# Optimization experiments

Measured on AMD Instinct MI355X. Metric: run time of the kernel, lower is better.

Reference implementation:

```python
import jax, jax.numpy as jnp
import numpy as np

B, T, D_IN, D, K, H, BAND = 4, 1536, 512, 512, 2, 8, 24
DH = D // H
ALPHA, BETA, EPS = 6.0, 0.5, 1e-5


def _ln(x, g, b):
    m = x.mean(-1, keepdims=True)
    v = ((x - m) ** 2).mean(-1, keepdims=True)
    return (x - m) / jnp.sqrt(v + EPS) * g + b


def setup_inputs() -> dict:
    key = jax.random.key(0)
    ks = jax.random.split(key, 16)
    sc = 0.02
    inp = {
        "x_m": jax.random.normal(ks[0], (B, T, D_IN), jnp.float32),
        "A": jax.random.uniform(ks[1], (B, T, K), jnp.float32),
        "W_in": jax.random.normal(ks[2], (D_IN, D), jnp.float32) * sc,
        "b_in": jnp.zeros((D,), jnp.float32),
        "ln_q_g": jnp.ones((D,), jnp.float32), "ln_q_b": jnp.zeros((D,), jnp.float32),
        "ln_kv_g": jnp.ones((D,), jnp.float32), "ln_kv_b": jnp.zeros((D,), jnp.float32),
        "Wq": jax.random.normal(ks[3], (D, D), jnp.float32) * sc,
        "bq": jnp.zeros((D,), jnp.float32),
        "Wk": jax.random.normal(ks[4], (D, D), jnp.float32) * sc,
        "bk": jnp.zeros((D,), jnp.float32),
        "Wv": jax.random.normal(ks[5], (D, D), jnp.float32) * sc,
        "bv": jnp.zeros((D,), jnp.float32),
        "Wo": jax.random.normal(ks[6], (D, D), jnp.float32) * sc,
        "bo": jnp.zeros((D,), jnp.float32),
        "ln_f_g": jnp.ones((D,), jnp.float32), "ln_f_b": jnp.zeros((D,), jnp.float32),
        "W1": jax.random.normal(ks[7], (D, 4 * D), jnp.float32) * sc,
        "b1": jnp.zeros((4 * D,), jnp.float32),
        "W2": jax.random.normal(ks[8], (4 * D, D), jnp.float32) * sc,
        "b2": jnp.zeros((D,), jnp.float32),
        "ln_s_g": jnp.ones((D,), jnp.float32), "ln_s_b": jnp.zeros((D,), jnp.float32),
        "spk_tags": jax.random.normal(ks[9], (K, D), jnp.float32) / np.sqrt(D),
    }
    return inp


def reference(x_m, A, W_in, b_in, ln_q_g, ln_q_b, ln_kv_g, ln_kv_b,
              Wq, bq, Wk, bk, Wv, bv, Wo, bo,
              ln_f_g, ln_f_b, W1, b1, W2, b2, ln_s_g, ln_s_b, spk_tags):
    X = x_m @ W_in + b_in                      # [B,T,D]
    W_hat = jax.nn.sigmoid(ALPHA * (A - BETA))  # [B,T,K] sigmoid gating

    # banded additive mask (|i-j| <= BAND allowed)
    idx = jnp.arange(T)
    allowed = jnp.abs(idx[:, None] - idx[None, :]) <= BAND
    mask = jnp.where(allowed, 0.0, -jnp.inf).astype(X.dtype)  # [T,T]

    # K/V come from the (shared) mixed memory X
    KV = _ln(X, ln_kv_g, ln_kv_b)
    k_p = (KV @ Wk + bk).reshape(B, T, H, DH)
    v_p = (KV @ Wv + bv).reshape(B, T, H, DH)

    streams = []
    for kk in range(K):
        Xk = X * W_hat[..., kk:kk + 1]
        Q = _ln(Xk, ln_q_g, ln_q_b)
        q = (Q @ Wq + bq).reshape(B, T, H, DH)
        scores = jnp.einsum('bthd,bshd->bhts', q, k_p) / np.sqrt(DH) + mask
        p = jax.nn.softmax(scores, axis=-1)
        y = jnp.einsum('bhts,bshd->bthd', p, v_p).reshape(B, T, D) @ Wo + bo
        y = Xk + y                              # residual after attention
        h = _ln(y, ln_f_g, ln_f_b)
        h = jax.nn.gelu(h @ W1 + b1, approximate=False) @ W2 + b2
        out_k = y + h + spk_tags[kk]            # ffn residual + speaker tag
        out_k = _ln(out_k, ln_s_g, ln_s_b)      # per-stream LayerNorm
        streams.append(out_k)
    return jnp.concatenate(streams, axis=1)    # [B, K*T, D]
```

## Files before the change

kernel.cpp:

```cpp
#include <hip/hip_runtime.h>
#include <hip/hip_bf16.h>
#include <math.h>

#define B_    4
#define T_    1536
#define DIN_  512
#define D_    512
#define K_    2
#define H_    8
#define BAND_ 24
#define DH_   64
#define M_    (B_*T_)
#define M2_   (2*M_)
#define ALPHA_ 6.0f
#define BETA_  0.5f
#define EPS_   1e-5f

using bf8  = __attribute__((ext_vector_type(8))) short;
using f32x4 = __attribute__((ext_vector_type(4))) float;

__device__ __forceinline__ void async_copy16(const void* g, void* l) {
  __builtin_amdgcn_global_load_lds(
      (const __attribute__((address_space(1))) unsigned int*)g,
      (__attribute__((address_space(3))) unsigned int*)l, 16, 0, 0);
}

__device__ __forceinline__ short f2bf(float v) {
  __hip_bfloat16 h = (__hip_bfloat16)v;
  return *(short*)&h;
}
__device__ __forceinline__ float bf2f(short s) {
  union { unsigned u; float f; } c;
  c.u = ((unsigned)(unsigned short)s) << 16;
  return c.f;
}
__device__ __forceinline__ int swz64(int row, int col) {
  return (col & ~63) | ((((col >> 3) ^ row) & 7) << 3) | (col & 7);
}
__device__ __forceinline__ float fast_gelu(float x) {
  const float t = fmaf(0.1029504013f, x * x, 2.3021170686f);
  const float e = __builtin_amdgcn_exp2f(x * t);
  const float r = __builtin_amdgcn_rcpf(e + 1.0f);
  return fmaf(-x, r, x);
}
__device__ __forceinline__ float wave_sum(float s) {
#pragma unroll
  for (int o = 1; o < 64; o <<= 1) s += __shfl_xor(s, o);
  return s;
}

template<int BM, int BN, int NI, int NJ, int FLAGS>
__global__ __launch_bounds__(256) void gemm_bt_t(
    const short* __restrict__ A, const short* __restrict__ Bt,
    const float* __restrict__ bias, const void* __restrict__ res,
    const float* __restrict__ tag2,
    void* __restrict__ Cout, int M, int N, int Kd, int gx) {
  __shared__ short lA[BM * 64];
  __shared__ short lB[BN * 64];
  const int gy   = gridDim.x / gx;
  const int xcd  = blockIdx.x & 7;
  const int seq  = blockIdx.x >> 3;
  const int rpx  = gy >> 3;
  const int by   = xcd * rpx + seq / gx;
  const int bx   = seq % gx;
  const int tid  = threadIdx.x;
  const int wave = tid >> 6, lane = tid & 63;
  const int block_m = by * BM, block_n = bx * BN;
  const int wm = (wave & 1) * (BM / 2), wn = (wave >> 1) * (BN / 2);
  const int l15 = lane & 15, quad = lane >> 4, l7 = lane & 7;
  f32x4 acc[NI][NJ] = {};

  for (int k0 = 0; k0 < Kd; k0 += 64) {
    __syncthreads();
#pragma unroll
    for (int i = 0; i < BM / 32; ++i) {
      const int cb = wave * (BM * 2) + i * 64;
      const int c  = cb + lane;
      async_copy16(A + (size_t)(block_m + (c >> 3)) * Kd + k0 + (c & 7) * 8,
                   &lA[cb * 8]);
    }
#pragma unroll
    for (int i = 0; i < BN / 32; ++i) {
      const int cb = wave * (BN * 2) + i * 64;
      const int c  = cb + lane;
      async_copy16(Bt + (size_t)(block_n + (c >> 3)) * Kd + k0 + (c & 7) * 8,
                   &lB[cb * 8]);
    }
    __syncthreads();
#pragma unroll
    for (int ks = 0; ks < 2; ++ks) {
      bf8 af[NI], bfr[NJ];
#pragma unroll
      for (int i = 0; i < NI; ++i)
        af[i] = *(const bf8*)&lA[(wm + i * 16 + l15) * 64 + (((ks * 4 + quad) ^ l7) << 3)];
#pragma unroll
      for (int j = 0; j < NJ; ++j)
        bfr[j] = *(const bf8*)&lB[(wn + j * 16 + l15) * 64 + (((ks * 4 + quad) ^ l7) << 3)];
#pragma unroll
      for (int i = 0; i < NI; ++i)
#pragma unroll
        for (int j = 0; j < NJ; ++j)
          acc[i][j] = __builtin_amdgcn_mfma_f32_16x16x32_bf16(bfr[j], af[i], acc[i][j], 0, 0, 0);
    }
  }

  const int half = M >> 1;
#pragma unroll
  for (int i = 0; i < NI; ++i) {
    const int row  = block_m + wm + i * 16 + l15;
    const size_t rowN = (size_t)row * N;
    const int toff = (row >= half) ? N : 0;
#pragma unroll
    for (int j = 0; j < NJ; ++j) {
      const int colb = block_n + wn + j * 16 + quad * 4;
      const float4 bb = *(const float4*)&bias[colb];
      float v0 = acc[i][j][0] + bb.x;
      float v1 = acc[i][j][1] + bb.y;
      float v2 = acc[i][j][2] + bb.z;
      float v3 = acc[i][j][3] + bb.w;
      if constexpr (FLAGS & 8) {
        const short4 rv = *(const short4*)&((const short*)res)[rowN + colb];
        v0 += bf2f(rv.x); v1 += bf2f(rv.y); v2 += bf2f(rv.z); v3 += bf2f(rv.w);
      }
      if constexpr (FLAGS & 16) {
        const float4 rv = *(const float4*)&((const float*)res)[rowN + colb];
        v0 += rv.x; v1 += rv.y; v2 += rv.z; v3 += rv.w;
      }
      if constexpr (FLAGS & 32) {
        const float4 tg = *(const float4*)&tag2[toff + colb];
        v0 += tg.x; v1 += tg.y; v2 += tg.z; v3 += tg.w;
      }
      if constexpr (FLAGS & 1) {
        v0 = fast_gelu(v0); v1 = fast_gelu(v1);
        v2 = fast_gelu(v2); v3 = fast_gelu(v3);
      }
      if constexpr (FLAGS & 2) {
        const int oc = (FLAGS & 4) ? swz64(row, colb) : colb;
        short4 o;
        o.x = f2bf(v0); o.y = f2bf(v1); o.z = f2bf(v2); o.w = f2bf(v3);
        *(short4*)&((short*)Cout)[rowN + oc] = o;
      } else {
        float4 o; o.x = v0; o.y = v1; o.z = v2; o.w = v3;
        *(float4*)&((float*)Cout)[rowN + colb] = o;
      }
    }
  }
}

__device__ __forceinline__ void tconv_tile(const float* __restrict__ W,
                                           short* __restrict__ Wt, int K, int N,
                                           int bx, int by, int tid, float (*s)[33]) {
  const int tx = tid & 31, ty = tid >> 5;
  const int k0 = by * 32, n0 = bx * 32;
#pragma unroll
  for (int r = 0; r < 4; ++r)
    s[ty * 4 + r][tx] = W[(size_t)(k0 + ty * 4 + r) * N + n0 + tx];
  __syncthreads();
#pragma unroll
  for (int r = 0; r < 4; ++r) {
    const int n = n0 + ty * 4 + r;
    Wt[(size_t)n * K + swz64(n, k0 + tx)] = f2bf(s[tx][ty * 4 + r]);
  }
}

__global__ __launch_bounds__(256) void prep_k(
    const float* __restrict__ x_m, short* __restrict__ xb,
    const float* __restrict__ W_in, short* __restrict__ WtIn,
    const float* __restrict__ Wq,  short* __restrict__ WtQ,
    const float* __restrict__ Wk,  const float* __restrict__ Wv,
    short* __restrict__ WtKV,
    const float* __restrict__ Wo,  short* __restrict__ WtO,
    const float* __restrict__ W1,  short* __restrict__ Wt1,
    const float* __restrict__ W2,  short* __restrict__ Wt2,
    const float* __restrict__ bk,  const float* __restrict__ bv,
    float* __restrict__ bkv) {
  __shared__ float s[32][33];
  const int blk = blockIdx.x, tid = threadIdx.x;
  if (blk < 3072) {
    const int e = (blk * 256 + tid) * 4;
    const int row = e >> 9, col = e & 511;
    const float4 v = *(const float4*)&x_m[e];
    short4 o;
    o.x = f2bf(v.x); o.y = f2bf(v.y); o.z = f2bf(v.z); o.w = f2bf(v.w);
    *(short4*)&xb[((size_t)row << 9) | swz64(row, col)] = o;
  } else if (blk < 3328) {
    const int t = blk - 3072; tconv_tile(W_in, WtIn, DIN_, D_, t & 15, t >> 4, tid, s);
  } else if (blk < 3584) {
    const int t = blk - 3328; tconv_tile(Wq, WtQ, D_, D_, t & 15, t >> 4, tid, s);
  } else if (blk < 3840) {
    const int t = blk - 3584; tconv_tile(Wk, WtKV, D_, D_, t & 15, t >> 4, tid, s);
  } else if (blk < 4096) {
    const int t = blk - 3840; tconv_tile(Wv, WtKV + (size_t)D_ * D_, D_, D_, t & 15, t >> 4, tid, s);
  } else if (blk < 4352) {
    const int t = blk - 4096; tconv_tile(Wo, WtO, D_, D_, t & 15, t >> 4, tid, s);
  } else if (blk < 5376) {
    const int t = blk - 4352; tconv_tile(W1, Wt1, D_, 4 * D_, t & 63, t >> 6, tid, s);
  } else if (blk < 6400) {
    const int t = blk - 5376; tconv_tile(W2, Wt2, 4 * D_, D_, t & 15, t >> 4, tid, s);
  } else {
    const int i = (blk - 6400) * 256 + tid;
    bkv[i] = (i < D_) ? bk[i] : bv[i - D_];
  }
}

__global__ __launch_bounds__(256) void ln_bf_k(const short* __restrict__ in,
                                               const float* __restrict__ g,
                                               const float* __restrict__ b,
                                               short* __restrict__ out) {
  const int row  = blockIdx.x * 4 + (threadIdx.x >> 6);
  const int lane = threadIdx.x & 63;
  const int c0   = lane * 8;
  const bf8 xv = *(const bf8*)&in[(size_t)row * D_ + c0];
  float v[8];
  float s = 0.0f;
#pragma unroll
  for (int e = 0; e < 8; ++e) { v[e] = bf2f(xv[e]); s += v[e]; }
  const float mean = wave_sum(s) * (1.0f / D_);
  float s2 = 0.0f;
#pragma unroll
  for (int e = 0; e < 8; ++e) { v[e] -= mean; s2 += v[e] * v[e]; }
  const float inv = rsqrtf(wave_sum(s2) * (1.0f / D_) + EPS_);
  const float4 g0 = *(const float4*)&g[c0];
  const float4 g1 = *(const float4*)&g[c0 + 4];
  const float4 b0 = *(const float4*)&b[c0];
  const float4 b1 = *(const float4*)&b[c0 + 4];
  bf8 o;
  o[0] = f2bf(v[0] * inv * g0.x + b0.x);
  o[1] = f2bf(v[1] * inv * g0.y + b0.y);
  o[2] = f2bf(v[2] * inv * g0.z + b0.z);
  o[3] = f2bf(v[3] * inv * g0.w + b0.w);
  o[4] = f2bf(v[4] * inv * g1.x + b1.x);
  o[5] = f2bf(v[5] * inv * g1.y + b1.y);
  o[6] = f2bf(v[6] * inv * g1.z + b1.z);
  o[7] = f2bf(v[7] * inv * g1.w + b1.w);
  *(bf8*)&out[(size_t)row * D_ + swz64(row, c0)] = o;
}

__global__ __launch_bounds__(256) void scale_ln_k(
    const short* __restrict__ X, const float* __restrict__ Ain,
    const float* __restrict__ g, const float* __restrict__ b,
    short* __restrict__ Xk, short* __restrict__ out) {
  const int row  = blockIdx.x * 4 + (threadIdx.x >> 6);
  const int lane = threadIdx.x & 63;
  const int c0   = lane * 8;
  const int kk = row / M_, rm = row % M_;
  const float a = Ain[(size_t)rm * K_ + kk];
  const float w = __builtin_amdgcn_rcpf(1.0f + __expf(-ALPHA_ * (a - BETA_)));
  const bf8 xv = *(const bf8*)&X[(size_t)rm * D_ + c0];
  float v[8];
  float s = 0.0f;
  bf8 xo;
#pragma unroll
  for (int e = 0; e < 8; ++e) {
    v[e] = bf2f(xv[e]) * w;
    xo[e] = f2bf(v[e]);
    s += v[e];
  }
  *(bf8*)&Xk[(size_t)row * D_ + c0] = xo;
  const float mean = wave_sum(s) * (1.0f / D_);
  float s2 = 0.0f;
#pragma unroll
  for (int e = 0; e < 8; ++e) { v[e] -= mean; s2 += v[e] * v[e]; }
  const float inv = rsqrtf(wave_sum(s2) * (1.0f / D_) + EPS_);
  const float4 g0 = *(const float4*)&g[c0];
  const float4 g1 = *(const float4*)&g[c0 + 4];
  const float4 b0 = *(const float4*)&b[c0];
  const float4 b1 = *(const float4*)&b[c0 + 4];
  bf8 o;
  o[0] = f2bf(v[0] * inv * g0.x + b0.x);
  o[1] = f2bf(v[1] * inv * g0.y + b0.y);
  o[2] = f2bf(v[2] * inv * g0.z + b0.z);
  o[3] = f2bf(v[3] * inv * g0.w + b0.w);
  o[4] = f2bf(v[4] * inv * g1.x + b1.x);
  o[5] = f2bf(v[5] * inv * g1.y + b1.y);
  o[6] = f2bf(v[6] * inv * g1.z + b1.z);
  o[7] = f2bf(v[7] * inv * g1.w + b1.w);
  *(bf8*)&out[(size_t)row * D_ + swz64(row, c0)] = o;
}

__global__ __launch_bounds__(256) void final_ln_k(
    const short* __restrict__ t2, const float* __restrict__ g,
    const float* __restrict__ b, float* __restrict__ out) {
  const int row  = blockIdx.x * 4 + (threadIdx.x >> 6);
  const int lane = threadIdx.x & 63;
  const int c0   = lane * 8;
  const int kk = row / M_, rm = row % M_;
  const int bb_ = rm / T_, t = rm % T_;
  const size_t orow = (size_t)bb_ * (K_ * T_) + (size_t)kk * T_ + t;
  const bf8 xv = *(const bf8*)&t2[(size_t)row * D_ + c0];
  float v[8];
  float s = 0.0f;
#pragma unroll
  for (int e = 0; e < 8; ++e) { v[e] = bf2f(xv[e]); s += v[e]; }
  const float mean = wave_sum(s) * (1.0f / D_);
  float s2 = 0.0f;
#pragma unroll
  for (int e = 0; e < 8; ++e) { v[e] -= mean; s2 += v[e] * v[e]; }
  const float inv = rsqrtf(wave_sum(s2) * (1.0f / D_) + EPS_);
  const float4 g0 = *(const float4*)&g[c0];
  const float4 g1 = *(const float4*)&g[c0 + 4];
  const float4 b0 = *(const float4*)&b[c0];
  const float4 b1 = *(const float4*)&b[c0 + 4];
  float4 o0, o1;
  o0.x = v[0] * inv * g0.x + b0.x;
  o0.y = v[1] * inv * g0.y + b0.y;
  o0.z = v[2] * inv * g0.z + b0.z;
  o0.w = v[3] * inv * g0.w + b0.w;
  o1.x = v[4] * inv * g1.x + b1.x;
  o1.y = v[5] * inv * g1.y + b1.y;
  o1.z = v[6] * inv * g1.z + b1.z;
  o1.w = v[7] * inv * g1.w + b1.w;
  *(float4*)&out[orow * D_ + c0]     = o0;
  *(float4*)&out[orow * D_ + c0 + 4] = o1;
}

#define QT_  64
#define KT_  (QT_ + 2 * BAND_)
#define SKQ_ 72
#define STV_ 136
__global__ __launch_bounds__(256) void attn_mfma_k(
    const short* __restrict__ q, const short* __restrict__ KVp,
    short* __restrict__ out) {
  __shared__ short sK[KT_ * SKQ_];
  __shared__ short sQ[QT_ * SKQ_];
  __shared__ short sVt[DH_ * STV_];
  __shared__ short sP[4][16 * SKQ_];
  const int t0 = blockIdx.x * QT_;
  const int h  = blockIdx.y;
  const int z  = blockIdx.z;
  const int b  = z % B_;
  const int tid = threadIdx.x;
  const int wave = tid >> 6, lane = tid & 63;
  const int rr = tid >> 5, c2 = tid & 31;

  for (int r0 = 0; r0 < KT_; r0 += 8) {
    const int r = r0 + rr;
    const int s = t0 - BAND_ + r;
    short2 kv = {0, 0}, vv = {0, 0};
    if (s >= 0 && s < T_) {
      const size_t g = (size_t)(b * T_ + s) * (2 * D_) + h * DH_ + c2 * 2;
      kv = *(const short2*)&KVp[g];
      vv = *(const short2*)&KVp[g + D_];
    }
    *(short2*)&sK[r * SKQ_ + c2 * 2] = kv;
    sVt[(c2 * 2)     * STV_ + r] = vv.x;
    sVt[(c2 * 2 + 1) * STV_ + r] = vv.y;
  }
  for (int r0 = 0; r0 < QT_; r0 += 8) {
    const int r = r0 + rr;
    const size_t g = (size_t)(z * T_ + t0 + r) * D_ + h * DH_ + c2 * 2;
    *(short2*)&sQ[r * SKQ_ + c2 * 2] = *(const short2*)&q[g];
  }
  __syncthreads();

  const int qg  = wave * 16;
  const int l15 = lane & 15, quad = lane >> 4;

  bf8 qa0 = *(const bf8*)&sQ[(qg + l15) * SKQ_ + quad * 8];
  bf8 qa1 = *(const bf8*)&sQ[(qg + l15) * SKQ_ + 32 + quad * 8];
  f32x4 acc[4];
#pragma unroll
  for (int j = 0; j < 4; ++j) {
    const bf8 kb0 = *(const bf8*)&sK[(qg + j * 16 + l15) * SKQ_ + quad * 8];
    const bf8 kb1 = *(const bf8*)&sK[(qg + j * 16 + l15) * SKQ_ + 32 + quad * 8];
    f32x4 z4 = {0.f, 0.f, 0.f, 0.f};
    acc[j] = __builtin_amdgcn_mfma_f32_16x16x32_bf16(qa0, kb0, z4, 0, 0, 0);
    acc[j] = __builtin_amdgcn_mfma_f32_16x16x32_bf16(qa1, kb1, acc[j], 0, 0, 0);
  }

#pragma unroll
  for (int reg = 0; reg < 4; ++reg) {
    const int i = quad * 4 + reg;
    float sc[4];
    float mx = -1e30f;
#pragma unroll
    for (int j = 0; j < 4; ++j) {
      const int c = j * 16 + l15;
      const int s = t0 + qg - BAND_ + c;
      const int rel = c - i;
      const bool valid = (rel >= 0) && (rel <= 2 * BAND_) && (s >= 0) && (s < T_);
      sc[j] = valid ? acc[j][reg] * 0.125f : -1e30f;
      mx = fmaxf(mx, sc[j]);
    }
    for (int o = 1; o < 16; o <<= 1) mx = fmaxf(mx, __shfl_xor(mx, o));
    float p[4], se = 0.0f;
#pragma unroll
    for (int j = 0; j < 4; ++j) {
      p[j] = (sc[j] > -1e29f) ? __expf(sc[j] - mx) : 0.0f;
      se += p[j];
    }
    for (int o = 1; o < 16; o <<= 1) se += __shfl_xor(se, o);
    const float inv = __builtin_amdgcn_rcpf(se);
#pragma unroll
    for (int j = 0; j < 4; ++j)
      sP[wave][i * SKQ_ + j * 16 + l15] = f2bf(p[j] * inv);
  }

  const bf8 pa0 = *(const bf8*)&sP[wave][l15 * SKQ_ + quad * 8];
  const bf8 pa1 = *(const bf8*)&sP[wave][l15 * SKQ_ + 32 + quad * 8];
  f32x4 oacc[4] = {};
#pragma unroll
  for (int dt = 0; dt < 4; ++dt) {
    const bf8 vb0 = *(const bf8*)&sVt[(dt * 16 + l15) * STV_ + qg + quad * 8];
    const bf8 vb1 = *(const bf8*)&sVt[(dt * 16 + l15) * STV_ + qg + 32 + quad * 8];
    oacc[dt] = __builtin_amdgcn_mfma_f32_16x16x32_bf16(pa0, vb0, oacc[dt], 0, 0, 0);
    oacc[dt] = __builtin_amdgcn_mfma_f32_16x16x32_bf16(pa1, vb1, oacc[dt], 0, 0, 0);
  }
#pragma unroll
  for (int dt = 0; dt < 4; ++dt)
#pragma unroll
    for (int reg = 0; reg < 4; ++reg) {
      const int i = quad * 4 + reg;
      const int row = t0 + qg + i;
      const int col = h * DH_ + dt * 16 + l15;
      out[(size_t)(z * T_ + row) * D_ + swz64(row, col)] = f2bf(oacc[dt][reg]);
    }
}

extern "C" void kernel_launch(void* const* d_in, const int* in_sizes, int n_in,
                              void* d_out, int out_size, void* d_ws, size_t ws_size,
                              hipStream_t stream) {
  const float* x_m    = (const float*)d_in[0];
  const float* A      = (const float*)d_in[1];
  const float* W_in   = (const float*)d_in[2];
  const float* b_in   = (const float*)d_in[3];
  const float* ln_q_g = (const float*)d_in[4];
  const float* ln_q_b = (const float*)d_in[5];
  const float* ln_kv_g= (const float*)d_in[6];
  const float* ln_kv_b= (const float*)d_in[7];
  const float* Wq     = (const float*)d_in[8];
  const float* bq     = (const float*)d_in[9];
  const float* Wk     = (const float*)d_in[10];
  const float* bk     = (const float*)d_in[11];
  const float* Wv     = (const float*)d_in[12];
  const float* bv     = (const float*)d_in[13];
  const float* Wo     = (const float*)d_in[14];
  const float* bo     = (const float*)d_in[15];
  const float* ln_f_g = (const float*)d_in[16];
  const float* ln_f_b = (const float*)d_in[17];
  const float* W1     = (const float*)d_in[18];
  const float* b1     = (const float*)d_in[19];
  const float* W2     = (const float*)d_in[20];
  const float* b2     = (const float*)d_in[21];
  const float* ln_s_g = (const float*)d_in[22];
  const float* ln_s_b = (const float*)d_in[23];
  const float* tags   = (const float*)d_in[24];
  float* out = (float*)d_out;

  const size_t MD = (size_t)M_ * D_;
  float* bkv = (float*)d_ws;
  short* X    = (short*)(bkv + 1024);
  short* Xk2  = X    + MD;
  short* LNb2 = Xk2  + 2 * MD;
  short* qb2  = LNb2 + 2 * MD;
  short* KVpb = qb2  + 2 * MD;
  short* T2b  = KVpb + 2 * MD;
  short* H1b  = T2b  + 2 * MD;
  short* WtIn = H1b + (size_t)M2_ * 4 * D_;
  short* WtQ  = WtIn + (size_t)D_ * DIN_;
  short* WtKV = WtQ  + (size_t)D_ * D_;
  short* WtO  = WtKV + (size_t)2 * D_ * D_;
  short* Wt1  = WtO  + (size_t)D_ * D_;
  short* Wt2  = Wt1  + (size_t)4 * D_ * D_;
  short* xb   = qb2;
  short* KVb  = LNb2;

  prep_k<<<6404, 256, 0, stream>>>(x_m, xb, W_in, WtIn, Wq, WtQ, Wk, Wv, WtKV,
                                   Wo, WtO, W1, Wt1, W2, Wt2, bk, bv, bkv);

  gemm_bt_t<128,64,4,2, 2><<<(D_/64) * (M_/128), 256, 0, stream>>>(
      xb, WtIn, b_in, nullptr, nullptr, X, M_, D_, DIN_, D_/64);
  ln_bf_k<<<M_/4, 256, 0, stream>>>(X, ln_kv_g, ln_kv_b, KVb);
  gemm_bt_t<128,128,4,4, 2><<<((2*D_)/128) * (M_/128), 256, 0, stream>>>(
      KVb, WtKV, bkv, nullptr, nullptr, KVpb, M_, 2*D_, D_, (2*D_)/128);

  scale_ln_k<<<M2_/4, 256, 0, stream>>>(X, A, ln_q_g, ln_q_b, Xk2, LNb2);
  gemm_bt_t<128,128,4,4, 2><<<(D_/128) * (M2_/128), 256, 0, stream>>>(
      LNb2, WtQ, bq, nullptr, nullptr, qb2, M2_, D_, D_, D_/128);
  attn_mfma_k<<<dim3(T_/QT_, H_, B_*K_), 256, 0, stream>>>(qb2, KVpb, LNb2);
  gemm_bt_t<128,128,4,4, 2|8><<<(D_/128) * (M2_/128), 256, 0, stream>>>(
      LNb2, WtO, bo, Xk2, nullptr, Xk2, M2_, D_, D_, D_/128);
  ln_bf_k<<<M2_/4, 256, 0, stream>>>(Xk2, ln_f_g, ln_f_b, LNb2);
  gemm_bt_t<128,64,4,2, 1|2|4><<<((4*D_)/64) * (M2_/128), 256, 0, stream>>>(
      LNb2, Wt1, b1, nullptr, nullptr, H1b, M2_, 4*D_, D_, (4*D_)/64);
  gemm_bt_t<128,64,4,2, 2|8|32><<<(D_/64) * (M2_/128), 256, 0, stream>>>(
      H1b, Wt2, b2, Xk2, tags, T2b, M2_, D_, 4*D_, D_/64);
  final_ln_k<<<M2_/4, 256, 0, stream>>>(T2b, ln_s_g, ln_s_b, out);
}
```

Baseline: 308.0 us.

## Merge KV and Q layernorm kernels and run KV/Q projections in one launch

Combines the KV layernorm and the gated Q layernorm into a single kernel over 3*M rows. Runs the KV and Q projection GEMMs as one dual-grid launch sharing a 128x128 core, which cuts two launches and lets both GEMMs fill the GPU together. KVb moves to a separate workspace region so it no longer aliases LNb2. The W1 GEMM tile also grows from 128x64 to 128x128. The new GEMM core assumes K=512, row-major bias and no swizzle on its output, and it adds workspace usage.

After: 302.7 us. About the same (-1.7%).

```diff
diff --git a/kernel.cpp b/kernel.cpp
--- a/kernel.cpp
+++ b/kernel.cpp
@@ -144,6 +144,91 @@
         *(float4*)&((float*)Cout)[rowN + colb] = o;
       }
     }
+  }
+}
+
+__device__ __forceinline__ void gemm128_core(
+    const short* __restrict__ A, const short* __restrict__ Bt,
+    const float* __restrict__ bias, short* __restrict__ Cout,
+    int N, int Kd, int bid, int gx, int gy, short* lA, short* lB) {
+  const int xcd  = bid & 7;
+  const int seq  = bid >> 3;
+  const int rpx  = gy >> 3;
+  const int by   = xcd * rpx + seq / gx;
+  const int bx   = seq % gx;
+  const int tid  = threadIdx.x;
+  const int wave = tid >> 6, lane = tid & 63;
+  const int block_m = by * 128, block_n = bx * 128;
+  const int wm = (wave & 1) * 64, wn = (wave >> 1) * 64;
+  const int l15 = lane & 15, quad = lane >> 4, l7 = lane & 7;
+  f32x4 acc[4][4] = {};
+
+  for (int k0 = 0; k0 < Kd; k0 += 64) {
+    __syncthreads();
+#pragma unroll
+    for (int i = 0; i < 4; ++i) {
+      const int cb = wave * 256 + i * 64;
+      const int c  = cb + lane;
+      async_copy16(A + (size_t)(block_m + (c >> 3)) * Kd + k0 + (c & 7) * 8,
+                   &lA[cb * 8]);
+    }
+#pragma unroll
+    for (int i = 0; i < 4; ++i) {
+      const int cb = wave * 256 + i * 64;
+      const int c  = cb + lane;
+      async_copy16(Bt + (size_t)(block_n + (c >> 3)) * Kd + k0 + (c & 7) * 8,
+                   &lB[cb * 8]);
+    }
+    __syncthreads();
+#pragma unroll
+    for (int ks = 0; ks < 2; ++ks) {
+      bf8 af[4], bfr[4];
+#pragma unroll
+      for (int i = 0; i < 4; ++i)
+        af[i] = *(const bf8*)&lA[(wm + i * 16 + l15) * 64 + (((ks * 4 + quad) ^ l7) << 3)];
+#pragma unroll
+      for (int j = 0; j < 4; ++j)
+        bfr[j] = *(const bf8*)&lB[(wn + j * 16 + l15) * 64 + (((ks * 4 + quad) ^ l7) << 3)];
+#pragma unroll
+      for (int i = 0; i < 4; ++i)
+#pragma unroll
+        for (int j = 0; j < 4; ++j)
+          acc[i][j] = __builtin_amdgcn_mfma_f32_16x16x32_bf16(bfr[j], af[i], acc[i][j], 0, 0, 0);
+    }
+  }
+
+#pragma unroll
+  for (int i = 0; i < 4; ++i) {
+    const int row  = block_m + wm + i * 16 + l15;
+    const size_t rowN = (size_t)row * N;
+#pragma unroll
+    for (int j = 0; j < 4; ++j) {
+      const int colb = block_n + wn + j * 16 + quad * 4;
+      const float4 bb = *(const float4*)&bias[colb];
+      short4 o;
+      o.x = f2bf(acc[i][j][0] + bb.x);
+      o.y = f2bf(acc[i][j][1] + bb.y);
+      o.z = f2bf(acc[i][j][2] + bb.z);
+      o.w = f2bf(acc[i][j][3] + bb.w);
+      *(short4*)&Cout[rowN + colb] = o;
+    }
+  }
+}
+
+__global__ __launch_bounds__(256) void gemm_dual_k(
+    const short* __restrict__ A0, const short* __restrict__ Bt0,
+    const float* __restrict__ bias0, short* __restrict__ C0, int N0, int nb0, int gx0,
+    const short* __restrict__ A1, const short* __restrict__ Bt1,
+    const float* __restrict__ bias1, short* __restrict__ C1, int N1, int gx1) {
+  __shared__ short lA[128 * 64];
+  __shared__ short lB[128 * 64];
+  const int bid = blockIdx.x;
+  if (bid < nb0) {
+    gemm128_core(A0, Bt0, bias0, C0, N0, D_, bid, gx0, nb0 / gx0, lA, lB);
+  } else {
+    const int b1 = bid - nb0;
+    const int nb1 = gridDim.x - nb0;
+    gemm128_core(A1, Bt1, bias1, C1, N1, D_, b1, gx1, nb1 / gx1, lA, lB);
   }
 }
 
@@ -236,46 +321,73 @@
   *(bf8*)&out[(size_t)row * D_ + swz64(row, c0)] = o;
 }
 
-__global__ __launch_bounds__(256) void scale_ln_k(
+__global__ __launch_bounds__(256) void ln_gate_k(
     const short* __restrict__ X, const float* __restrict__ Ain,
-    const float* __restrict__ g, const float* __restrict__ b,
-    short* __restrict__ Xk, short* __restrict__ out) {
+    const float* __restrict__ gkv, const float* __restrict__ bkvp,
+    const float* __restrict__ gq, const float* __restrict__ bqp,
+    short* __restrict__ KVb, short* __restrict__ Xk, short* __restrict__ LNq) {
   const int row  = blockIdx.x * 4 + (threadIdx.x >> 6);
   const int lane = threadIdx.x & 63;
   const int c0   = lane * 8;
-  const int kk = row / M_, rm = row % M_;
-  const float a = Ain[(size_t)rm * K_ + kk];
-  const float w = __builtin_amdgcn_rcpf(1.0f + __expf(-ALPHA_ * (a - BETA_)));
-  const bf8 xv = *(const bf8*)&X[(size_t)rm * D_ + c0];
   float v[8];
   float s = 0.0f;
-  bf8 xo;
-#pragma unroll
-  for (int e = 0; e < 8; ++e) {
-    v[e] = bf2f(xv[e]) * w;
-    xo[e] = f2bf(v[e]);
-    s += v[e];
-  }
-  *(bf8*)&Xk[(size_t)row * D_ + c0] = xo;
-  const float mean = wave_sum(s) * (1.0f / D_);
-  float s2 = 0.0f;
-#pragma unroll
-  for (int e = 0; e < 8; ++e) { v[e] -= mean; s2 += v[e] * v[e]; }
-  const float inv = rsqrtf(wave_sum(s2) * (1.0f / D_) + EPS_);
-  const float4 g0 = *(const float4*)&g[c0];
-  const float4 g1 = *(const float4*)&g[c0 + 4];
-  const float4 b0 = *(const float4*)&b[c0];
-  const float4 b1 = *(const float4*)&b[c0 + 4];
-  bf8 o;
-  o[0] = f2bf(v[0] * inv * g0.x + b0.x);
-  o[1] = f2bf(v[1] * inv * g0.y + b0.y);
-  o[2] = f2bf(v[2] * inv * g0.z + b0.z);
-  o[3] = f2bf(v[3] * inv * g0.w + b0.w);
-  o[4] = f2bf(v[4] * inv * g1.x + b1.x);
-  o[5] = f2bf(v[5] * inv * g1.y + b1.y);
-  o[6] = f2bf(v[6] * inv * g1.z + b1.z);
-  o[7] = f2bf(v[7] * inv * g1.w + b1.w);
-  *(bf8*)&out[(size_t)row * D_ + swz64(row, c0)] = o;
+  if (row < M_) {
+    const bf8 xv = *(const bf8*)&X[(size_t)row * D_ + c0];
+#pragma unroll
+    for (int e = 0; e < 8; ++e) { v[e] = bf2f(xv[e]); s += v[e]; }
+    const float mean = wave_sum(s) * (1.0f / D_);
+    float s2 = 0.0f;
+#pragma unroll
+    for (int e = 0; e < 8; ++e) { v[e] -= mean; s2 += v[e] * v[e]; }
+    const float inv = rsqrtf(wave_sum(s2) * (1.0f / D_) + EPS_);
+    const float4 g0 = *(const float4*)&gkv[c0];
+    const float4 g1 = *(const float4*)&gkv[c0 + 4];
+    const float4 b0 = *(const float4*)&bkvp[c0];
+    const float4 b1 = *(const float4*)&bkvp[c0 + 4];
+    bf8 o;
+    o[0] = f2bf(v[0] * inv * g0.x + b0.x);
+    o[1] = f2bf(v[1] * inv * g0.y + b0.y);
+    o[2] = f2bf(v[2] * inv * g0.z + b0.z);
+    o[3] = f2bf(v[3] * inv * g0.w + b0.w);
+    o[4] = f2bf(v[4] * inv * g1.x + b1.x);
+    o[5] = f2bf(v[5] * inv * g1.y + b1.y);
+    o[6] = f2bf(v[6] * inv * g1.z + b1.z);
+    o[7] = f2bf(v[7] * inv * g1.w + b1.w);
+    *(bf8*)&KVb[(size_t)row * D_ + swz64(row, c0)] = o;
+  } else {
+    const int r2 = row - M_;
+    const int kk = r2 / M_, rm = r2 % M_;
+    const float a = Ain[(size_t)rm * K_ + kk];
+    const float w = __builtin_amdgcn_rcpf(1.0f + __expf(-ALPHA_ * (a - BETA_)));
+    const bf8 xv = *(const bf8*)&X[(size_t)rm * D_ + c0];
+    bf8 xo;
+#pragma unroll
+    for (int e = 0; e < 8; ++e) {
+      v[e] = bf2f(xv[e]) * w;
+      xo[e] = f2bf(v[e]);
+      s += v[e];
+    }
+    *(bf8*)&Xk[(size_t)r2 * D_ + c0] = xo;
+    const float mean = wave_sum(s) * (1.0f / D_);
+    float s2 = 0.0f;
+#pragma unroll
+    for (int e = 0; e < 8; ++e) { v[e] -= mean; s2 += v[e] * v[e]; }
+    const float inv = rsqrtf(wave_sum(s2) * (1.0f / D_) + EPS_);
+    const float4 g0 = *(const float4*)&gq[c0];
+    const float4 g1 = *(const float4*)&gq[c0 + 4];
+    const float4 b0 = *(const float4*)&bqp[c0];
+    const float4 b1 = *(const float4*)&bqp[c0 + 4];
+    bf8 o;
+    o[0] = f2bf(v[0] * inv * g0.x + b0.x);
+    o[1] = f2bf(v[1] * inv * g0.y + b0.y);
+    o[2] = f2bf(v[2] * inv * g0.z + b0.z);
+    o[3] = f2bf(v[3] * inv * g0.w + b0.w);
+    o[4] = f2bf(v[4] * inv * g1.x + b1.x);
+    o[5] = f2bf(v[5] * inv * g1.y + b1.y);
+    o[6] = f2bf(v[6] * inv * g1.z + b1.z);
+    o[7] = f2bf(v[7] * inv * g1.w + b1.w);
+    *(bf8*)&LNq[(size_t)r2 * D_ + swz64(r2, c0)] = o;
+  }
 }
 
 __global__ __launch_bounds__(256) void final_ln_k(
@@ -462,27 +574,28 @@
   short* WtO  = WtKV + (size_t)2 * D_ * D_;
   short* Wt1  = WtO  + (size_t)D_ * D_;
   short* Wt2  = Wt1  + (size_t)4 * D_ * D_;
+  short* KVb  = Wt2  + (size_t)4 * D_ * D_;
   short* xb   = qb2;
-  short* KVb  = LNb2;
 
   prep_k<<<6404, 256, 0, stream>>>(x_m, xb, W_in, WtIn, Wq, WtQ, Wk, Wv, WtKV,
                                    Wo, WtO, W1, Wt1, W2, Wt2, bk, bv, bkv);
 
   gemm_bt_t<128,64,4,2, 2><<<(D_/64) * (M_/128), 256, 0, stream>>>(
       xb, WtIn, b_in, nullptr, nullptr, X, M_, D_, DIN_, D_/64);
-  ln_bf_k<<<M_/4, 256, 0, stream>>>(X, ln_kv_g, ln_kv_b, KVb);
-  gemm_bt_t<128,128,4,4, 2><<<((2*D_)/128) * (M_/128), 256, 0, stream>>>(
-      KVb, WtKV, bkv, nullptr, nullptr, KVpb, M_, 2*D_, D_, (2*D_)/128);
-
-  scale_ln_k<<<M2_/4, 256, 0, stream>>>(X, A, ln_q_g, ln_q_b, Xk2, LNb2);
-  gemm_bt_t<128,128,4,4, 2><<<(D_/128) * (M2_/128), 256, 0, stream>>>(
-      LNb2, WtQ, bq, nullptr, nullptr, qb2, M2_, D_, D_, D_/128);
+
+  ln_gate_k<<<(3 * M_) / 4, 256, 0, stream>>>(
+      X, A, ln_kv_g, ln_kv_b, ln_q_g, ln_q_b, KVb, Xk2, LNb2);
+
+  gemm_dual_k<<<768, 256, 0, stream>>>(
+      KVb, WtKV, bkv, KVpb, 2 * D_, ((2*D_)/128) * (M_/128), (2*D_)/128,
+      LNb2, WtQ, bq, qb2, D_, D_/128);
+
   attn_mfma_k<<<dim3(T_/QT_, H_, B_*K_), 256, 0, stream>>>(qb2, KVpb, LNb2);
   gemm_bt_t<128,128,4,4, 2|8><<<(D_/128) * (M2_/128), 256, 0, stream>>>(
       LNb2, WtO, bo, Xk2, nullptr, Xk2, M2_, D_, D_, D_/128);
   ln_bf_k<<<M2_/4, 256, 0, stream>>>(Xk2, ln_f_g, ln_f_b, LNb2);
-  gemm_bt_t<128,64,4,2, 1|2|4><<<((4*D_)/64) * (M2_/128), 256, 0, stream>>>(
-      LNb2, Wt1, b1, nullptr, nullptr, H1b, M2_, 4*D_, D_, (4*D_)/64);
+  gemm_bt_t<128,128,4,4, 1|2|4><<<((4*D_)/128) * (M2_/128), 256, 0, stream>>>(
+      LNb2, Wt1, b1, nullptr, nullptr, H1b, M2_, 4*D_, D_, (4*D_)/128);
   gemm_bt_t<128,64,4,2, 2|8|32><<<(D_/64) * (M2_/128), 256, 0, stream>>>(
       H1b, Wt2, b2, Xk2, tags, T2b, M2_, D_, 4*D_, D_/64);
   final_ln_k<<<M2_/4, 256, 0, stream>>>(T2b, ln_s_g, ln_s_b, out);
```
